# Kernel optimization log

Measured on AMD Instinct MI355X. Metric: run time of the kernel, lower is better.

## Reference

```python
import jax, jax.numpy as jnp
import numpy as np

NEG_RATIO = 3.0
IOU_THR = 0.5
ALPHA = 1.0


def _cxcywh_to_xyxy(b):
    return jnp.concatenate([b[..., :2] - b[..., 2:] / 2, b[..., :2] + b[..., 2:] / 2], -1)


def _box_iou(a, b):  # a: [G,4] xyxy, b: [A,4] xyxy -> [G,A]
    lt = jnp.maximum(a[:, None, :2], b[None, :, :2])
    rb = jnp.minimum(a[:, None, 2:], b[None, :, 2:])
    wh = jnp.clip(rb - lt, 0.0)
    inter = wh[..., 0] * wh[..., 1]
    area_a = (a[:, 2] - a[:, 0]) * (a[:, 3] - a[:, 1])
    area_b = (b[:, 2] - b[:, 0]) * (b[:, 3] - b[:, 1])
    return inter / (area_a[:, None] + area_b[None, :] - inter)


def _encode(gt, anc):  # both cxcywh, last dim 4
    g_cxcy = (gt[..., :2] - anc[..., :2]) / anc[..., 2:]
    g_wh = jnp.log(gt[..., 2:]) - jnp.log(anc[..., 2:])
    return jnp.concatenate([g_cxcy, g_wh], -1)


def _match_one(boxes, labels, anchors):
    # boxes: [G,4] cxcywh, labels: [G] int, anchors: [A,4] cxcywh -> [A,5]
    ious = _box_iou(_cxcywh_to_xyxy(boxes), _cxcywh_to_xyxy(anchors))  # [G,A]
    best_gt_ov = ious.max(0)
    best_gt_idx = ious.argmax(0)  # [A]
    over = best_gt_ov > IOU_THR  # [A]
    lab_f = labels.astype(anchors.dtype)
    # anchors over threshold take their best gt, encoded w.r.t. that anchor
    enc_per_anchor = _encode(boxes[best_gt_idx], anchors)  # [A,4]
    ph = jnp.where(over[:, None],
                   jnp.concatenate([enc_per_anchor, lab_f[best_gt_idx][:, None]], -1),
                   0.0)  # [A,5]
    # every gt also claims its best anchor
    best_prior_idx = ious.argmax(1)  # [G]
    enc_best = _encode(boxes, anchors[best_prior_idx])  # [G,4]
    y2 = jnp.concatenate([enc_best, lab_f[:, None]], -1)
    return ph.at[best_prior_idx].set(y2)


def _multibox_loss(loc_pred, conf_pred, anchors, gt_boxes, gt_labels):
    B, A, C = conf_pred.shape
    target = jax.vmap(_match_one, in_axes=(0, 0, None))(gt_boxes, gt_labels, anchors)  # [B,A,5]
    pos = (target[:, :, 4:5] > 0).astype(loc_pred.dtype)  # [B,A,1]
    num_pos = pos.sum(axis=1, keepdims=True)  # [B,1,1]
    N = pos.sum()
    # smooth L1 on masked locations (beta=1), sum reduction
    d = pos * loc_pred - pos * target[:, :, :4]
    ad = jnp.abs(d)
    loc_loss = jnp.where(ad < 1.0, 0.5 * d * d, ad - 0.5).sum()
    # hard negative mining
    num_neg = jnp.minimum(NEG_RATIO * num_pos, A - 1)  # [B,1,1]
    lse = jax.scipy.special.logsumexp(conf_pred, axis=-1, keepdims=True)  # [B,A,1]
    idx01 = (target[:, :, 4:5] != 0).astype(jnp.int32)  # faithful: gathers class 0 or 1
    gathered = jnp.take_along_axis(conf_pred, idx01, axis=-1)  # [B,A,1]
    cls_l = (lse - gathered) * (1.0 - pos)  # zero-out positives
    order = jnp.argsort(-cls_l, axis=1)  # descending sort indices
    rank = jnp.argsort(order, axis=1)  # rank of each box's loss
    neg_mask = rank < num_neg
    sampled = jnp.logical_or(pos > 0, neg_mask)  # [B,A,1]
    s = sampled.astype(conf_pred.dtype)
    logits = (s * conf_pred).reshape(-1, C)
    labels_ce = (s * target[:, :, 4:5]).reshape(-1).astype(jnp.int32)
    lse2 = jax.scipy.special.logsumexp(logits, axis=-1)
    picked = jnp.take_along_axis(logits, labels_ce[:, None], axis=1)[:, 0]
    cls_loss = (lse2 - picked).sum()
    return (loc_loss + ALPHA * cls_loss) / N


def setup_inputs() -> dict:
    key = jax.random.key(0)
    k1, k2, k3, k4, k5, k6, k7 = jax.random.split(key, 7)
    B, A, C, G = 64, 8732, 81, 32
    loc_pred = jax.random.normal(k1, (B, A, 4), jnp.float32)
    conf_pred = jax.random.normal(k2, (B, A, C), jnp.float32)
    anc_cxcy = jax.random.uniform(k3, (A, 2), jnp.float32)
    anc_wh = jax.random.uniform(k4, (A, 2), jnp.float32) * 0.48 + 0.02
    anchors = jnp.concatenate([anc_cxcy, anc_wh], -1)
    gt_cxcy = jax.random.uniform(k5, (B, G, 2), jnp.float32) * 0.8 + 0.1
    gt_wh = jax.random.uniform(k6, (B, G, 2), jnp.float32) * 0.35 + 0.05
    gt_boxes = jnp.concatenate([gt_cxcy, gt_wh], -1)
    gt_labels = jax.random.randint(k7, (B, G), 0, C - 1, jnp.int32) + 1  # labels in 1..C-1
    return {"loc_pred": loc_pred, "conf_pred": conf_pred, "anchors": anchors,
            "gt_boxes": gt_boxes, "gt_labels": gt_labels}


def reference(loc_pred, conf_pred, anchors, gt_boxes, gt_labels):
    return _multibox_loss(loc_pred, conf_pred, anchors, gt_boxes, gt_labels)
```

## Files before the change

kernel.cpp:

```cpp
#include <hip/hip_runtime.h>
#include <math.h>

#pragma clang fp contract(off)

#define BB 64
#define AA 8732
#define CC 81
#define GG 32
#define A_BLOCKS 35
#define KC_GRID 1536
#define KA1_BLOCKS (BB*A_BLOCKS)
#define KA2_BLOCKS (BB*GG/4)
#define TOT_BLOCKS (KC_GRID+KA1_BLOCKS+KA2_BLOCKS)
#define ROWS_PC 64
#define KC_CHUNKS (BB*AA/ROWS_PC)
#define CHUNK_F4 (ROWS_PC*81/4)


__device__ __forceinline__ void iou_upd(const float4 an, int a,
    float gx1, float gy1, float gx2, float gy2, float gar2,
    float& bi, float& bu, int& ba)
{
    float ax1 = an.x - an.z / 2.0f, ay1 = an.y - an.w / 2.0f;
    float ax2 = an.x + an.z / 2.0f, ay2 = an.y + an.w / 2.0f;
    float aar = (ax2 - ax1) * (ay2 - ay1);
    float ltx = fmaxf(gx1, ax1), lty = fmaxf(gy1, ay1);
    float rbx = fminf(gx2, ax2), rby = fminf(gy2, ay2);
    float w = fmaxf(rbx - ltx, 0.0f), h = fmaxf(rby - lty, 0.0f);
    float inter = w * h;
    float uni = gar2 + aar - inter;
    if (inter * bu > bi * uni) { bi = inter; bu = uni; ba = a; }
}

__global__ __launch_bounds__(256) void kAC(const float* __restrict__ anchors,
    const float* __restrict__ gt_boxes, const float* __restrict__ conf,
    unsigned char* __restrict__ bestg, unsigned int* __restrict__ bestp,
    float* __restrict__ cls_l, unsigned int* __restrict__ ticket,
    double* __restrict__ btot_acc, int* __restrict__ np_acc)
{
    __shared__ float buf[ROWS_PC * 81];
    int tid = threadIdx.x;
    if (blockIdx.x == 0 && tid == 0) {
        *ticket = 0u; *btot_acc = 0.0; *np_acc = 0;
    }
    if (blockIdx.x < KC_GRID) {
        const float4* __restrict__ src4 = (const float4*)conf;
        float4* buf4 = (float4*)buf;
        float4 r0, r1, r2, r3, r4, r5;
        int c0 = blockIdx.x;
        {
            size_t b4 = (size_t)c0 * CHUNK_F4;
            r0 = src4[b4 + tid];        r1 = src4[b4 + tid + 256];
            r2 = src4[b4 + tid + 512];  r3 = src4[b4 + tid + 768];
            r4 = src4[b4 + tid + 1024];
            if (tid < 16) r5 = src4[b4 + tid + 1280];
            buf4[tid] = r0; buf4[tid + 256] = r1; buf4[tid + 512] = r2;
            buf4[tid + 768] = r3; buf4[tid + 1024] = r4;
            if (tid < 16) buf4[tid + 1280] = r5;
        }
        for (int c = c0; c < KC_CHUNKS; c += KC_GRID) {
            int nx = c + KC_GRID;
            __syncthreads();
            if (nx < KC_CHUNKS) {
                size_t b4 = (size_t)nx * CHUNK_F4;
                r0 = src4[b4 + tid];        r1 = src4[b4 + tid + 256];
                r2 = src4[b4 + tid + 512];  r3 = src4[b4 + tid + 768];
                r4 = src4[b4 + tid + 1024];
                if (tid < 16) r5 = src4[b4 + tid + 1280];
            }
            {
                int r = tid >> 2, q = tid & 3;
                const float* row = buf + r * 81;
                int kstart = (q == 0) ? 0 : 21 + (q - 1) * 20;
                float s = 0.0f;
#pragma unroll
                for (int k = 0; k < 20; ++k) s += __expf(row[kstart + k]);
                if (q == 0) s += __expf(row[20]);
                s += __shfl_xor(s, 1);
                s += __shfl_xor(s, 2);
                if (q == 0)
                    cls_l[c * ROWS_PC + r] = __logf(s) - row[0];
            }
            if (nx < KC_CHUNKS) {
                __syncthreads();
                buf4[tid] = r0; buf4[tid + 256] = r1; buf4[tid + 512] = r2;
                buf4[tid + 768] = r3; buf4[tid + 1024] = r4;
                if (tid < 16) buf4[tid + 1280] = r5;
            }
        }
    } else if (blockIdx.x < KC_GRID + KA1_BLOCKS) {
        float4* gco = (float4*)buf;
        float* gar = buf + 128;
        int blk = blockIdx.x - KC_GRID;
        int b = blk / A_BLOCKS, ca = blk % A_BLOCKS;
        int a = ca * 256 + tid;
        if (tid < GG) {
            float4 gb = ((const float4*)gt_boxes)[b * GG + tid];
            float x1 = gb.x - gb.z / 2.0f, y1 = gb.y - gb.w / 2.0f;
            float x2 = gb.x + gb.z / 2.0f, y2 = gb.y + gb.w / 2.0f;
            gco[tid] = make_float4(x1, y1, x2, y2);
            gar[tid] = (x2 - x1) * (y2 - y1);
        }
        __syncthreads();
        if (a >= AA) return;
        float4 an = ((const float4*)anchors)[a];
        float ax1 = an.x - an.z / 2.0f, ay1 = an.y - an.w / 2.0f;
        float ax2 = an.x + an.z / 2.0f, ay2 = an.y + an.w / 2.0f;
        float aar = (ax2 - ax1) * (ay2 - ay1);
        float bi = -1.0f, bu = 1.0f; int bgi = 0;
#pragma unroll
        for (int g = 0; g < GG; ++g) {
            float4 cbox = gco[g];
            float ltx = fmaxf(cbox.x, ax1), lty = fmaxf(cbox.y, ay1);
            float rbx = fminf(cbox.z, ax2), rby = fminf(cbox.w, ay2);
            float w = fmaxf(rbx - ltx, 0.0f), h = fmaxf(rby - lty, 0.0f);
            float inter = w * h;
            float uni = gar[g] + aar - inter;
            if (inter * bu > bi * uni) { bi = inter; bu = uni; bgi = g; }
        }
        bestg[b * AA + a] = (2.0f * bi > bu) ? (unsigned char)bgi : (unsigned char)0xFF;
    } else {
        int wv = tid >> 6, lane = tid & 63;
        int pair = (blockIdx.x - KC_GRID - KA1_BLOCKS) * 4 + wv;
        int b = pair >> 5, g = pair & 31;
        float4 gb = ((const float4*)gt_boxes)[b * GG + g];
        float gx1 = gb.x - gb.z / 2.0f, gy1 = gb.y - gb.w / 2.0f;
        float gx2 = gb.x + gb.z / 2.0f, gy2 = gb.y + gb.w / 2.0f;
        float gar2 = (gx2 - gx1) * (gy2 - gy1);
        const float4* __restrict__ A4 = (const float4*)anchors;
        float bi = -1.0f, bu = 1.0f; int ba = 0;
        for (int k0 = 0; k0 < 136; k0 += 8) {
            int a0 = lane + 64 * k0;
            float4 v0 = A4[a0];
            float4 v1 = A4[a0 + 64];
            float4 v2 = A4[a0 + 128];
            float4 v3 = A4[a0 + 192];
            float4 v4 = A4[a0 + 256];
            float4 v5 = A4[a0 + 320];
            float4 v6 = A4[a0 + 384];
            float4 v7 = A4[a0 + 448];
            iou_upd(v0, a0,       gx1, gy1, gx2, gy2, gar2, bi, bu, ba);
            iou_upd(v1, a0 + 64,  gx1, gy1, gx2, gy2, gar2, bi, bu, ba);
            iou_upd(v2, a0 + 128, gx1, gy1, gx2, gy2, gar2, bi, bu, ba);
            iou_upd(v3, a0 + 192, gx1, gy1, gx2, gy2, gar2, bi, bu, ba);
            iou_upd(v4, a0 + 256, gx1, gy1, gx2, gy2, gar2, bi, bu, ba);
            iou_upd(v5, a0 + 320, gx1, gy1, gx2, gy2, gar2, bi, bu, ba);
            iou_upd(v6, a0 + 384, gx1, gy1, gx2, gy2, gar2, bi, bu, ba);
            iou_upd(v7, a0 + 448, gx1, gy1, gx2, gy2, gar2, bi, bu, ba);
        }
        if (lane < 28) {
            int a = 8704 + lane;
            iou_upd(A4[a], a, gx1, gy1, gx2, gy2, gar2, bi, bu, ba);
        }
#pragma unroll
        for (int off = 32; off > 0; off >>= 1) {
            float oi = __shfl_down(bi, off);
            float ou = __shfl_down(bu, off);
            int   oa = __shfl_down(ba, off);
            float p1 = oi * bu, p2 = bi * ou;
            bool take = (p1 > p2) || ((p1 == p2) && (oa < ba));
            if (take) { bi = oi; bu = ou; ba = oa; }
        }
        if (lane == 0) bestp[pair] = (unsigned int)ba;
    }
}

__global__ __launch_bounds__(1024, 4) void kBE(const float* __restrict__ anchors,
    const float* __restrict__ gt_boxes, const int* __restrict__ gt_labels,
    const float* __restrict__ loc_pred, const unsigned char* __restrict__ bestg,
    const unsigned int* __restrict__ bestp, const float* __restrict__ cls_l,
    const float* __restrict__ conf, unsigned int* __restrict__ ticket,
    double* __restrict__ btot_acc, int* __restrict__ np_acc,
    float* __restrict__ out)
{
    int b = blockIdx.x, tid = threadIdx.x, lane = tid & 63;
    __shared__ unsigned int cl[AA];
    __shared__ unsigned char slab[AA];
    __shared__ unsigned int hist[256];
    __shared__ float gcx[GG], gcy[GG], gw[GG], gh[GG];
    __shared__ int glab[GG];
    __shared__ unsigned int bp[GG];
    __shared__ double red_d[16], red_p[16];
    __shared__ int red_i[16];
    __shared__ unsigned int red_u[16];
    __shared__ unsigned int sh_prefix, sh_remaining;
    __shared__ int sh_np;
    __shared__ double sh_loc, sh_pc;

    if (tid < GG) {
        float4 gb = ((const float4*)gt_boxes)[b * GG + tid];
        gcx[tid] = gb.x; gcy[tid] = gb.y; gw[tid] = gb.z; gh[tid] = gb.w;
        glab[tid] = gt_labels[b * GG + tid];
        bp[tid] = bestp[b * GG + tid];
    }
    __syncthreads();

    double lsum = 0.0, pc = 0.0; int pcount = 0;
    for (int a = tid; a < AA; a += 1024) {
        int gf = -1;
#pragma unroll
        for (int g = 0; g < GG; ++g)
            if (bp[g] == (unsigned int)a) gf = g;
        int gsel;
        if (gf >= 0) gsel = gf;
        else {
            unsigned char bg = bestg[b * AA + a];
            gsel = (bg == 0xFF) ? -1 : (int)bg;
        }
        int lab = 0;
        if (gsel >= 0) {
            lab = glab[gsel];
            float4 an = ((const float4*)anchors)[a];
            float e0 = (gcx[gsel] - an.x) / an.z;
            float e1 = (gcy[gsel] - an.y) / an.w;
            float e2 = logf(gw[gsel]) - logf(an.z);
            float e3 = logf(gh[gsel]) - logf(an.w);
            float4 lp = ((const float4*)loc_pred)[b * AA + a];
            float d0 = lp.x - e0, d1 = lp.y - e1, d2 = lp.z - e2, d3 = lp.w - e3;
            float t = 0.0f, ad;
            ad = fabsf(d0); t += (ad < 1.0f) ? 0.5f * d0 * d0 : ad - 0.5f;
            ad = fabsf(d1); t += (ad < 1.0f) ? 0.5f * d1 * d1 : ad - 0.5f;
            ad = fabsf(d2); t += (ad < 1.0f) ? 0.5f * d2 * d2 : ad - 0.5f;
            ad = fabsf(d3); t += (ad < 1.0f) ? 0.5f * d3 * d3 : ad - 0.5f;
            lsum += (double)t;
            pcount++;
        }
        slab[a] = (unsigned char)lab;
        float sv = cls_l[b * AA + a];
        if (lab > 0) {
            size_t rowb = ((size_t)(b * AA + a)) * 81;
            pc += (double)(sv + conf[rowb] - conf[rowb + lab]);
            cl[a] = 0u;
        } else {
            cl[a] = __float_as_uint(fmaxf(sv, 0.0f));
        }
    }
#pragma unroll
    for (int off = 32; off > 0; off >>= 1) {
        lsum += __shfl_down(lsum, off);
        pc += __shfl_down(pc, off);
        pcount += __shfl_down(pcount, off);
    }
    if (lane == 0) { red_d[tid >> 6] = lsum; red_p[tid >> 6] = pc; red_i[tid >> 6] = pcount; }
    __syncthreads();
    if (tid == 0) {
        double L = 0.0, C = 0.0; int P = 0;
        for (int w = 0; w < 16; ++w) { L += red_d[w]; C += red_p[w]; P += red_i[w]; }
        sh_loc = L; sh_pc = C; sh_np = P;
        sh_prefix = 0u;
        sh_remaining = (unsigned int)min(3 * P, AA - 1);
    }
    __syncthreads();
    int np_ = sh_np;
    int k = min(3 * np_, AA - 1);

    double topk = 0.0;
    int p_t_pos = 0;
    if (k > 0) {
        for (int shift = 24; shift >= 0; shift -= 8) {
            if (tid < 256) hist[tid] = 0u;
            __syncthreads();
            unsigned int mask = (shift == 24) ? 0u : (0xFFFFFFFFu << (shift + 8));
            unsigned int pre = sh_prefix;
#pragma unroll
            for (int it = 0; it < 9; ++it) {
                int i = tid + it * 1024;
                bool in = (i < AA);
                unsigned int u = in ? cl[i] : 0u;
                bool act = in && ((u & mask) == pre);
                unsigned int d = (u >> shift) & 255u;
                unsigned long long actm = __ballot(act);
                while (actm) {
                    int src = __builtin_ctzll(actm);
                    unsigned int d0 = (unsigned int)__shfl((int)d, src);
                    unsigned long long m = __ballot(act && (d == d0));
                    int c = __popcll(m);
                    if (c < 8) break;
                    if (lane == src) atomicAdd(&hist[d0], (unsigned int)c);
                    actm &= ~m;
                }
                if ((actm >> lane) & 1ull) atomicAdd(&hist[d], 1u);
            }
            __syncthreads();
            if (tid < 64) {
                int l = tid;
                unsigned int h4 = hist[4 * l] + hist[4 * l + 1]
                                + hist[4 * l + 2] + hist[4 * l + 3];
                unsigned int S = h4;
#pragma unroll
                for (int off = 1; off < 64; off <<= 1) {
                    unsigned int o = __shfl_down(S, off);
                    S += (l + off < 64) ? o : 0u;
                }
                unsigned int rem = sh_remaining;
                unsigned long long ball = __ballot(S >= rem);
                int L = 63 - __clzll(ball);
                if (l == L) {
                    unsigned int rem2 = rem - (S - h4);
                    unsigned int c = 0;
                    for (int dd = 4 * L + 3; dd >= 4 * L; --dd) {
                        c += hist[dd];
                        if (c >= rem2) {
                            sh_prefix = pre | ((unsigned int)dd << shift);
                            sh_remaining = rem2 - (c - hist[dd]);
                            break;
                        }
                    }
                }
            }
            __syncthreads();
        }
        unsigned int vbits = sh_prefix;
        unsigned int myc = 0; double mys = 0.0;
        for (int i = tid; i < AA; i += 1024) {
            unsigned int u = cl[i];
            if (u > vbits) { myc++; mys += (double)__uint_as_float(u); }
        }
#pragma unroll
        for (int off = 32; off > 0; off >>= 1) {
            myc += __shfl_down(myc, off);
            mys += __shfl_down(mys, off);
        }
        if (lane == 0) { red_u[tid >> 6] = myc; red_d[tid >> 6] = mys; }
        __syncthreads();
        if (tid == 0) {
            unsigned int cnt_gt = 0; double sum_gt = 0.0;
            for (int w = 0; w < 16; ++w) { cnt_gt += red_u[w]; sum_gt += red_d[w]; }
            topk = sum_gt + (double)(k - (int)cnt_gt) * (double)__uint_as_float(vbits);
            if (vbits == 0u) {
                int t = k - (int)cnt_gt, c2 = 0;
                for (int i = 0; i < AA && c2 < t; ++i) {
                    if (cl[i] == 0u) { c2++; if (slab[i] > 0) p_t_pos++; }
                }
            }
        }
    }
    if (tid == 0) {
        int unsampled = AA - np_ - k + p_t_pos;
        double clsb = sh_pc + topk + (double)unsampled * (double)logf(81.0f);
        double myb = sh_loc + clsb;
        atomicAdd(btot_acc, myb);
        atomicAdd(np_acc, np_);
        __threadfence();
        unsigned int t = atomicAdd(ticket, 1u);
        if (t == BB - 1) {
            double tt = atomicAdd(btot_acc, 0.0);
            int nn = atomicAdd(np_acc, 0);
            out[0] = (float)(tt / (double)nn);
        }
    }
}

extern "C" void kernel_launch(void* const* d_in, const int* in_sizes, int n_in,
                              void* d_out, int out_size, void* d_ws, size_t ws_size,
                              hipStream_t stream) {
    (void)in_sizes; (void)n_in; (void)out_size; (void)ws_size;
    const float* loc_pred  = (const float*)d_in[0];
    const float* conf_pred = (const float*)d_in[1];
    const float* anchors   = (const float*)d_in[2];
    const float* gt_boxes  = (const float*)d_in[3];
    const int*   gt_labels = (const int*)d_in[4];

    char* ws = (char*)d_ws;
    unsigned int*  bestp    = (unsigned int*)(ws + 0);
    unsigned char* bestg    = (unsigned char*)(ws + 8192);
    float*         cls_l    = (float*)(ws + 567040);
    unsigned int*  ticket   = (unsigned int*)(ws + 2802432);
    double*        btot_acc = (double*)(ws + 2802440);
    int*           np_acc   = (int*)(ws + 2802448);

    kAC<<<TOT_BLOCKS, 256, 0, stream>>>(anchors, gt_boxes, conf_pred,
        bestg, bestp, cls_l, ticket, btot_acc, np_acc);
    kBE<<<BB, 1024, 0, stream>>>(anchors, gt_boxes, gt_labels, loc_pred,
        bestg, bestp, cls_l, conf_pred, ticket, btot_acc, np_acc, (float*)d_out);
}
```

Before: 314.2 us.

## Fuse match, softmax and loss stages into one kernel with per-batch ready counters

Merges the two kernels into a single persistent-style launch of 1024-thread blocks. The per-batch loss blocks spin on per-batch ready counters, which the log-sum-exp, best-gt and best-prior producer blocks increment. This lets loss work for early batches overlap with producers still running for later ones, and removes the kernel boundary. It also reshapes the producer work, with 16 threads per row for log-sum-exp and 1024-wide anchor blocks, and adds a small init kernel to zero the counters. The spin-wait relies on every producer block being scheduled before or alongside the waiting consumers; if they are not, it can deadlock or waste occupancy.

```diff
diff --git a/kernel.cpp b/kernel.cpp
--- a/kernel.cpp
+++ b/kernel.cpp
@@ -5,17 +5,35 @@
 
 #define BB 64
 #define AA 8732
-#define CC 81
 #define GG 32
-#define A_BLOCKS 35
-#define KC_GRID 1536
-#define KA1_BLOCKS (BB*A_BLOCKS)
-#define KA2_BLOCKS (BB*GG/4)
-#define TOT_BLOCKS (KC_GRID+KA1_BLOCKS+KA2_BLOCKS)
-#define ROWS_PC 64
-#define KC_CHUNKS (BB*AA/ROWS_PC)
-#define CHUNK_F4 (ROWS_PC*81/4)
-
+
+#define KC_GRID    768
+#define KC_CHUNKS  8732
+#define CHUNK_F4   1296
+#define KC_TRIPS   12
+#define KA1_PER    9
+#define KA1_BLOCKS (BB*KA1_PER)
+#define KA2_BLOCKS (BB*2)
+#define ROLE_A1    KC_GRID
+#define ROLE_A2    (KC_GRID+KA1_BLOCKS)
+#define ROLE_BE    (KC_GRID+KA1_BLOCKS+KA2_BLOCKS)
+#define TOT_BLOCKS (ROLE_BE+BB)
+
+
+struct BESmem {
+    unsigned int cl[AA];
+    unsigned int hist[256];
+    float gcx[GG], gcy[GG], gw[GG], gh[GG];
+    int glab[GG];
+    unsigned int bp[GG];
+    double red_d[16], red_p[16];
+    double sh_loc, sh_pc;
+    int red_i[16];
+    unsigned int red_u[16];
+    unsigned int sh_prefix, sh_remaining;
+    int sh_np;
+    unsigned char slab[AA];
+};
 
 __device__ __forceinline__ void iou_upd(const float4 an, int a,
     float gx1, float gy1, float gx2, float gy2, float gar2,
@@ -32,68 +50,92 @@
     if (inter * bu > bi * uni) { bi = inter; bu = uni; ba = a; }
 }
 
-__global__ __launch_bounds__(256) void kAC(const float* __restrict__ anchors,
-    const float* __restrict__ gt_boxes, const float* __restrict__ conf,
+__global__ __launch_bounds__(256) void kInit(unsigned int* __restrict__ z)
+{
+    for (int i = threadIdx.x; i < 1029; i += 256) z[i] = 0u;
+}
+
+__global__ __launch_bounds__(1024, 4) void kFused(
+    const float* __restrict__ loc_pred, const float* __restrict__ conf,
+    const float* __restrict__ anchors, const float* __restrict__ gt_boxes,
+    const int* __restrict__ gt_labels,
     unsigned char* __restrict__ bestg, unsigned int* __restrict__ bestp,
-    float* __restrict__ cls_l, unsigned int* __restrict__ ticket,
-    double* __restrict__ btot_acc, int* __restrict__ np_acc)
+    float* __restrict__ cls_l, unsigned int* __restrict__ ready,
+    unsigned int* __restrict__ ticket, double* __restrict__ btot_acc,
+    int* __restrict__ np_acc, float* __restrict__ out)
 {
-    __shared__ float buf[ROWS_PC * 81];
+    __shared__ __align__(16) unsigned char smem[sizeof(BESmem)];
     int tid = threadIdx.x;
-    if (blockIdx.x == 0 && tid == 0) {
-        *ticket = 0u; *btot_acc = 0.0; *np_acc = 0;
-    }
+
     if (blockIdx.x < KC_GRID) {
+        float* buf = (float*)smem;
+        float4* buf4 = (float4*)smem;
         const float4* __restrict__ src4 = (const float4*)conf;
-        float4* buf4 = (float4*)buf;
-        float4 r0, r1, r2, r3, r4, r5;
-        int c0 = blockIdx.x;
+        float4 r0, r1;
         {
-            size_t b4 = (size_t)c0 * CHUNK_F4;
-            r0 = src4[b4 + tid];        r1 = src4[b4 + tid + 256];
-            r2 = src4[b4 + tid + 512];  r3 = src4[b4 + tid + 768];
-            r4 = src4[b4 + tid + 1024];
-            if (tid < 16) r5 = src4[b4 + tid + 1280];
-            buf4[tid] = r0; buf4[tid + 256] = r1; buf4[tid + 512] = r2;
-            buf4[tid + 768] = r3; buf4[tid + 1024] = r4;
-            if (tid < 16) buf4[tid + 1280] = r5;
-        }
-        for (int c = c0; c < KC_CHUNKS; c += KC_GRID) {
+            size_t b4 = (size_t)blockIdx.x * CHUNK_F4;
+            r0 = src4[b4 + tid];
+            if (tid < CHUNK_F4 - 1024) r1 = src4[b4 + 1024 + tid];
+            buf4[tid] = r0;
+            if (tid < CHUNK_F4 - 1024) buf4[1024 + tid] = r1;
+        }
+        int pend = -1;
+        for (int t = 0; t < KC_TRIPS; ++t) {
+            int c = blockIdx.x + t * KC_GRID;
             int nx = c + KC_GRID;
+            bool hc = c < KC_CHUNKS, hn = nx < KC_CHUNKS;
             __syncthreads();
-            if (nx < KC_CHUNKS) {
+            if (pend >= 0) {
+                if (tid == 0) {
+                    __threadfence();
+                    int i1 = (pend * 64) / AA, i2 = (pend * 64 + 63) / AA;
+                    atomicAdd(&ready[i1 * 16], 1u);
+                    if (i2 != i1) atomicAdd(&ready[i2 * 16], 1u);
+                }
+                pend = -1;
+            }
+            if (hn) {
                 size_t b4 = (size_t)nx * CHUNK_F4;
-                r0 = src4[b4 + tid];        r1 = src4[b4 + tid + 256];
-                r2 = src4[b4 + tid + 512];  r3 = src4[b4 + tid + 768];
-                r4 = src4[b4 + tid + 1024];
-                if (tid < 16) r5 = src4[b4 + tid + 1280];
-            }
-            {
-                int r = tid >> 2, q = tid & 3;
+                r0 = src4[b4 + tid];
+                if (tid < CHUNK_F4 - 1024) r1 = src4[b4 + 1024 + tid];
+            }
+            if (hc) {
+                int r = tid >> 4, q = tid & 15;
                 const float* row = buf + r * 81;
-                int kstart = (q == 0) ? 0 : 21 + (q - 1) * 20;
-                float s = 0.0f;
-#pragma unroll
-                for (int k = 0; k < 20; ++k) s += __expf(row[kstart + k]);
-                if (q == 0) s += __expf(row[20]);
-                s += __shfl_xor(s, 1);
-                s += __shfl_xor(s, 2);
+                float s;
+                if (q == 0) {
+                    s = __expf(row[0]) + __expf(row[1]) + __expf(row[2])
+                      + __expf(row[3]) + __expf(row[4]) + __expf(row[5]);
+                } else {
+                    int ks = 6 + (q - 1) * 5;
+                    s = __expf(row[ks]) + __expf(row[ks + 1]) + __expf(row[ks + 2])
+                      + __expf(row[ks + 3]) + __expf(row[ks + 4]);
+                }
+                s += __shfl_xor(s, 1); s += __shfl_xor(s, 2);
+                s += __shfl_xor(s, 4); s += __shfl_xor(s, 8);
                 if (q == 0)
-                    cls_l[c * ROWS_PC + r] = __logf(s) - row[0];
-            }
-            if (nx < KC_CHUNKS) {
+                    cls_l[c * 64 + r] = __logf(s) - row[0];
+            }
+            if (hn) {
                 __syncthreads();
-                buf4[tid] = r0; buf4[tid + 256] = r1; buf4[tid + 512] = r2;
-                buf4[tid + 768] = r3; buf4[tid + 1024] = r4;
-                if (tid < 16) buf4[tid + 1280] = r5;
-            }
-        }
-    } else if (blockIdx.x < KC_GRID + KA1_BLOCKS) {
-        float4* gco = (float4*)buf;
-        float* gar = buf + 128;
-        int blk = blockIdx.x - KC_GRID;
-        int b = blk / A_BLOCKS, ca = blk % A_BLOCKS;
-        int a = ca * 256 + tid;
+                buf4[tid] = r0;
+                if (tid < CHUNK_F4 - 1024) buf4[1024 + tid] = r1;
+            }
+            if (hc) pend = c;
+        }
+        __syncthreads();
+        if (pend >= 0 && tid == 0) {
+            __threadfence();
+            int i1 = (pend * 64) / AA, i2 = (pend * 64 + 63) / AA;
+            atomicAdd(&ready[i1 * 16], 1u);
+            if (i2 != i1) atomicAdd(&ready[i2 * 16], 1u);
+        }
+    } else if (blockIdx.x < ROLE_A2) {
+        float4* gco = (float4*)smem;
+        float* gar = (float*)smem + 128;
+        int blk = blockIdx.x - ROLE_A1;
+        int b = blk / KA1_PER, ca = blk % KA1_PER;
+        int a = ca * 1024 + tid;
         if (tid < GG) {
             float4 gb = ((const float4*)gt_boxes)[b * GG + tid];
             float x1 = gb.x - gb.z / 2.0f, y1 = gb.y - gb.w / 2.0f;
@@ -102,26 +144,31 @@
             gar[tid] = (x2 - x1) * (y2 - y1);
         }
         __syncthreads();
-        if (a >= AA) return;
-        float4 an = ((const float4*)anchors)[a];
-        float ax1 = an.x - an.z / 2.0f, ay1 = an.y - an.w / 2.0f;
-        float ax2 = an.x + an.z / 2.0f, ay2 = an.y + an.w / 2.0f;
-        float aar = (ax2 - ax1) * (ay2 - ay1);
-        float bi = -1.0f, bu = 1.0f; int bgi = 0;
-#pragma unroll
-        for (int g = 0; g < GG; ++g) {
-            float4 cbox = gco[g];
-            float ltx = fmaxf(cbox.x, ax1), lty = fmaxf(cbox.y, ay1);
-            float rbx = fminf(cbox.z, ax2), rby = fminf(cbox.w, ay2);
-            float w = fmaxf(rbx - ltx, 0.0f), h = fmaxf(rby - lty, 0.0f);
-            float inter = w * h;
-            float uni = gar[g] + aar - inter;
-            if (inter * bu > bi * uni) { bi = inter; bu = uni; bgi = g; }
-        }
-        bestg[b * AA + a] = (2.0f * bi > bu) ? (unsigned char)bgi : (unsigned char)0xFF;
-    } else {
+        if (a < AA) {
+            float4 an = ((const float4*)anchors)[a];
+            float ax1 = an.x - an.z / 2.0f, ay1 = an.y - an.w / 2.0f;
+            float ax2 = an.x + an.z / 2.0f, ay2 = an.y + an.w / 2.0f;
+            float aar = (ax2 - ax1) * (ay2 - ay1);
+            float bi = -1.0f, bu = 1.0f; int bgi = 0;
+#pragma unroll
+            for (int g = 0; g < GG; ++g) {
+                float4 cbox = gco[g];
+                float ltx = fmaxf(cbox.x, ax1), lty = fmaxf(cbox.y, ay1);
+                float rbx = fminf(cbox.z, ax2), rby = fminf(cbox.w, ay2);
+                float w = fmaxf(rbx - ltx, 0.0f), h = fmaxf(rby - lty, 0.0f);
+                float inter = w * h;
+                float uni = gar[g] + aar - inter;
+                if (inter * bu > bi * uni) { bi = inter; bu = uni; bgi = g; }
+            }
+            bestg[b * AA + a] = (2.0f * bi > bu) ? (unsigned char)bgi
+                                                 : (unsigned char)0xFF;
+        }
+        __syncthreads();
+        if (tid == 0) { __threadfence(); atomicAdd(&ready[b * 16], 1u); }
+    } else if (blockIdx.x < ROLE_BE) {
         int wv = tid >> 6, lane = tid & 63;
-        int pair = (blockIdx.x - KC_GRID - KA1_BLOCKS) * 4 + wv;
+        int blk = blockIdx.x - ROLE_A2;
+        int pair = blk * 16 + wv;
         int b = pair >> 5, g = pair & 31;
         float4 gb = ((const float4*)gt_boxes)[b * GG + g];
         float gx1 = gb.x - gb.z / 2.0f, gy1 = gb.y - gb.w / 2.0f;
@@ -162,191 +209,182 @@
             if (take) { bi = oi; bu = ou; ba = oa; }
         }
         if (lane == 0) bestp[pair] = (unsigned int)ba;
-    }
-}
-
-__global__ __launch_bounds__(1024, 4) void kBE(const float* __restrict__ anchors,
-    const float* __restrict__ gt_boxes, const int* __restrict__ gt_labels,
-    const float* __restrict__ loc_pred, const unsigned char* __restrict__ bestg,
-    const unsigned int* __restrict__ bestp, const float* __restrict__ cls_l,
-    const float* __restrict__ conf, unsigned int* __restrict__ ticket,
-    double* __restrict__ btot_acc, int* __restrict__ np_acc,
-    float* __restrict__ out)
-{
-    int b = blockIdx.x, tid = threadIdx.x, lane = tid & 63;
-    __shared__ unsigned int cl[AA];
-    __shared__ unsigned char slab[AA];
-    __shared__ unsigned int hist[256];
-    __shared__ float gcx[GG], gcy[GG], gw[GG], gh[GG];
-    __shared__ int glab[GG];
-    __shared__ unsigned int bp[GG];
-    __shared__ double red_d[16], red_p[16];
-    __shared__ int red_i[16];
-    __shared__ unsigned int red_u[16];
-    __shared__ unsigned int sh_prefix, sh_remaining;
-    __shared__ int sh_np;
-    __shared__ double sh_loc, sh_pc;
-
-    if (tid < GG) {
-        float4 gb = ((const float4*)gt_boxes)[b * GG + tid];
-        gcx[tid] = gb.x; gcy[tid] = gb.y; gw[tid] = gb.z; gh[tid] = gb.w;
-        glab[tid] = gt_labels[b * GG + tid];
-        bp[tid] = bestp[b * GG + tid];
-    }
-    __syncthreads();
-
-    double lsum = 0.0, pc = 0.0; int pcount = 0;
-    for (int a = tid; a < AA; a += 1024) {
-        int gf = -1;
-#pragma unroll
-        for (int g = 0; g < GG; ++g)
-            if (bp[g] == (unsigned int)a) gf = g;
-        int gsel;
-        if (gf >= 0) gsel = gf;
-        else {
-            unsigned char bg = bestg[b * AA + a];
-            gsel = (bg == 0xFF) ? -1 : (int)bg;
-        }
-        int lab = 0;
-        if (gsel >= 0) {
-            lab = glab[gsel];
-            float4 an = ((const float4*)anchors)[a];
-            float e0 = (gcx[gsel] - an.x) / an.z;
-            float e1 = (gcy[gsel] - an.y) / an.w;
-            float e2 = logf(gw[gsel]) - logf(an.z);
-            float e3 = logf(gh[gsel]) - logf(an.w);
-            float4 lp = ((const float4*)loc_pred)[b * AA + a];
-            float d0 = lp.x - e0, d1 = lp.y - e1, d2 = lp.z - e2, d3 = lp.w - e3;
-            float t = 0.0f, ad;
-            ad = fabsf(d0); t += (ad < 1.0f) ? 0.5f * d0 * d0 : ad - 0.5f;
-            ad = fabsf(d1); t += (ad < 1.0f) ? 0.5f * d1 * d1 : ad - 0.5f;
-            ad = fabsf(d2); t += (ad < 1.0f) ? 0.5f * d2 * d2 : ad - 0.5f;
-            ad = fabsf(d3); t += (ad < 1.0f) ? 0.5f * d3 * d3 : ad - 0.5f;
-            lsum += (double)t;
-            pcount++;
-        }
-        slab[a] = (unsigned char)lab;
-        float sv = cls_l[b * AA + a];
-        if (lab > 0) {
-            size_t rowb = ((size_t)(b * AA + a)) * 81;
-            pc += (double)(sv + conf[rowb] - conf[rowb + lab]);
-            cl[a] = 0u;
-        } else {
-            cl[a] = __float_as_uint(fmaxf(sv, 0.0f));
-        }
-    }
-#pragma unroll
-    for (int off = 32; off > 0; off >>= 1) {
-        lsum += __shfl_down(lsum, off);
-        pc += __shfl_down(pc, off);
-        pcount += __shfl_down(pcount, off);
-    }
-    if (lane == 0) { red_d[tid >> 6] = lsum; red_p[tid >> 6] = pc; red_i[tid >> 6] = pcount; }
-    __syncthreads();
-    if (tid == 0) {
-        double L = 0.0, C = 0.0; int P = 0;
-        for (int w = 0; w < 16; ++w) { L += red_d[w]; C += red_p[w]; P += red_i[w]; }
-        sh_loc = L; sh_pc = C; sh_np = P;
-        sh_prefix = 0u;
-        sh_remaining = (unsigned int)min(3 * P, AA - 1);
-    }
-    __syncthreads();
-    int np_ = sh_np;
-    int k = min(3 * np_, AA - 1);
-
-    double topk = 0.0;
-    int p_t_pos = 0;
-    if (k > 0) {
-        for (int shift = 24; shift >= 0; shift -= 8) {
-            if (tid < 256) hist[tid] = 0u;
-            __syncthreads();
-            unsigned int mask = (shift == 24) ? 0u : (0xFFFFFFFFu << (shift + 8));
-            unsigned int pre = sh_prefix;
-#pragma unroll
-            for (int it = 0; it < 9; ++it) {
-                int i = tid + it * 1024;
-                bool in = (i < AA);
-                unsigned int u = in ? cl[i] : 0u;
-                bool act = in && ((u & mask) == pre);
-                unsigned int d = (u >> shift) & 255u;
-                unsigned long long actm = __ballot(act);
-                while (actm) {
-                    int src = __builtin_ctzll(actm);
-                    unsigned int d0 = (unsigned int)__shfl((int)d, src);
-                    unsigned long long m = __ballot(act && (d == d0));
-                    int c = __popcll(m);
-                    if (c < 8) break;
-                    if (lane == src) atomicAdd(&hist[d0], (unsigned int)c);
-                    actm &= ~m;
+        __syncthreads();
+        if (tid == 0) { __threadfence(); atomicAdd(&ready[b * 16], 1u); }
+    } else {
+        BESmem& S = *reinterpret_cast<BESmem*>(smem);
+        int b = blockIdx.x - ROLE_BE, lane = tid & 63;
+        if (tid == 0) {
+            unsigned int tgt = (unsigned int)(((AA * (b + 1) - 1) >> 6)
+                               - ((AA * b) >> 6) + 1 + KA1_PER + 2);
+            while (atomicAdd(&ready[b * 16], 0u) < tgt)
+                __builtin_amdgcn_s_sleep(2);
+            __threadfence();
+        }
+        __syncthreads();
+        if (tid < GG) {
+            float4 gb = ((const float4*)gt_boxes)[b * GG + tid];
+            S.gcx[tid] = gb.x; S.gcy[tid] = gb.y; S.gw[tid] = gb.z; S.gh[tid] = gb.w;
+            S.glab[tid] = gt_labels[b * GG + tid];
+            S.bp[tid] = bestp[b * GG + tid];
+        }
+        __syncthreads();
+
+        double lsum = 0.0, pc = 0.0; int pcount = 0;
+        for (int a = tid; a < AA; a += 1024) {
+            int gf = -1;
+#pragma unroll
+            for (int g = 0; g < GG; ++g)
+                if (S.bp[g] == (unsigned int)a) gf = g;
+            int gsel;
+            if (gf >= 0) gsel = gf;
+            else {
+                unsigned char bg = bestg[b * AA + a];
+                gsel = (bg == 0xFF) ? -1 : (int)bg;
+            }
+            int lab = 0;
+            if (gsel >= 0) {
+                lab = S.glab[gsel];
+                float4 an = ((const float4*)anchors)[a];
+                float e0 = (S.gcx[gsel] - an.x) / an.z;
+                float e1 = (S.gcy[gsel] - an.y) / an.w;
+                float e2 = logf(S.gw[gsel]) - logf(an.z);
+                float e3 = logf(S.gh[gsel]) - logf(an.w);
+                float4 lp = ((const float4*)loc_pred)[b * AA + a];
+                float d0 = lp.x - e0, d1 = lp.y - e1, d2 = lp.z - e2, d3 = lp.w - e3;
+                float t = 0.0f, ad;
+                ad = fabsf(d0); t += (ad < 1.0f) ? 0.5f * d0 * d0 : ad - 0.5f;
+                ad = fabsf(d1); t += (ad < 1.0f) ? 0.5f * d1 * d1 : ad - 0.5f;
+                ad = fabsf(d2); t += (ad < 1.0f) ? 0.5f * d2 * d2 : ad - 0.5f;
+                ad = fabsf(d3); t += (ad < 1.0f) ? 0.5f * d3 * d3 : ad - 0.5f;
+                lsum += (double)t;
+                pcount++;
+            }
+            S.slab[a] = (unsigned char)lab;
+            float sv = cls_l[b * AA + a];
+            if (lab > 0) {
+                size_t rowb = ((size_t)(b * AA + a)) * 81;
+                pc += (double)(sv + conf[rowb] - conf[rowb + lab]);
+                S.cl[a] = 0u;
+            } else {
+                S.cl[a] = __float_as_uint(fmaxf(sv, 0.0f));
+            }
+        }
+#pragma unroll
+        for (int off = 32; off > 0; off >>= 1) {
+            lsum += __shfl_down(lsum, off);
+            pc += __shfl_down(pc, off);
+            pcount += __shfl_down(pcount, off);
+        }
+        if (lane == 0) {
+            S.red_d[tid >> 6] = lsum; S.red_p[tid >> 6] = pc; S.red_i[tid >> 6] = pcount;
+        }
+        __syncthreads();
+        if (tid == 0) {
+            double L = 0.0, C = 0.0; int P = 0;
+            for (int w = 0; w < 16; ++w) { L += S.red_d[w]; C += S.red_p[w]; P += S.red_i[w]; }
+            S.sh_loc = L; S.sh_pc = C; S.sh_np = P;
+            S.sh_prefix = 0u;
+            S.sh_remaining = (unsigned int)min(3 * P, AA - 1);
+        }
+        __syncthreads();
+        int np_ = S.sh_np;
+        int k = min(3 * np_, AA - 1);
+
+        double topk = 0.0;
+        int p_t_pos = 0;
+        if (k > 0) {
+            for (int shift = 24; shift >= 0; shift -= 8) {
+                if (tid < 256) S.hist[tid] = 0u;
+                __syncthreads();
+                unsigned int mask = (shift == 24) ? 0u : (0xFFFFFFFFu << (shift + 8));
+                unsigned int pre = S.sh_prefix;
+#pragma unroll
+                for (int it = 0; it < 9; ++it) {
+                    int i = tid + it * 1024;
+                    bool in = (i < AA);
+                    unsigned int u = in ? S.cl[i] : 0u;
+                    bool act = in && ((u & mask) == pre);
+                    unsigned int d = (u >> shift) & 255u;
+                    unsigned long long actm = __ballot(act);
+                    while (actm) {
+                        int src = __builtin_ctzll(actm);
+                        unsigned int d0 = (unsigned int)__shfl((int)d, src);
+                        unsigned long long m = __ballot(act && (d == d0));
+                        int c = __popcll(m);
+                        if (c < 8) break;
+                        if (lane == src) atomicAdd(&S.hist[d0], (unsigned int)c);
+                        actm &= ~m;
+                    }
+                    if ((actm >> lane) & 1ull) atomicAdd(&S.hist[d], 1u);
                 }
-                if ((actm >> lane) & 1ull) atomicAdd(&hist[d], 1u);
-            }
-            __syncthreads();
-            if (tid < 64) {
-                int l = tid;
-                unsigned int h4 = hist[4 * l] + hist[4 * l + 1]
-                                + hist[4 * l + 2] + hist[4 * l + 3];
-                unsigned int S = h4;
-#pragma unroll
-                for (int off = 1; off < 64; off <<= 1) {
-                    unsigned int o = __shfl_down(S, off);
-                    S += (l + off < 64) ? o : 0u;
-                }
-                unsigned int rem = sh_remaining;
-                unsigned long long ball = __ballot(S >= rem);
-                int L = 63 - __clzll(ball);
-                if (l == L) {
-                    unsigned int rem2 = rem - (S - h4);
-                    unsigned int c = 0;
-                    for (int dd = 4 * L + 3; dd >= 4 * L; --dd) {
-                        c += hist[dd];
-                        if (c >= rem2) {
-                            sh_prefix = pre | ((unsigned int)dd << shift);
-                            sh_remaining = rem2 - (c - hist[dd]);
-                            break;
+                __syncthreads();
+                if (tid < 64) {
+                    int l = tid;
+                    unsigned int h4 = S.hist[4 * l] + S.hist[4 * l + 1]
+                                    + S.hist[4 * l + 2] + S.hist[4 * l + 3];
+                    unsigned int Ssum = h4;
+#pragma unroll
+                    for (int off = 1; off < 64; off <<= 1) {
+                        unsigned int o = __shfl_down(Ssum, off);
+                        Ssum += (l + off < 64) ? o : 0u;
+                    }
+                    unsigned int rem = S.sh_remaining;
+                    unsigned long long ball = __ballot(Ssum >= rem);
+                    int L = 63 - __clzll(ball);
+                    if (l == L) {
+                        unsigned int rem2 = rem - (Ssum - h4);
+                        unsigned int c = 0;
+                        for (int dd = 4 * L + 3; dd >= 4 * L; --dd) {
+                            c += S.hist[dd];
+                            if (c >= rem2) {
+                                S.sh_prefix = pre | ((unsigned int)dd << shift);
+                                S.sh_remaining = rem2 - (c - S.hist[dd]);
+                                break;
+                            }
                         }
                     }
                 }
-            }
+                __syncthreads();
+            }
+            unsigned int vbits = S.sh_prefix;
+            unsigned int myc = 0; double mys = 0.0;
+            for (int i = tid; i < AA; i += 1024) {
+                unsigned int u = S.cl[i];
+                if (u > vbits) { myc++; mys += (double)__uint_as_float(u); }
+            }
+#pragma unroll
+            for (int off = 32; off > 0; off >>= 1) {
+                myc += __shfl_down(myc, off);
+                mys += __shfl_down(mys, off);
+            }
+            if (lane == 0) { S.red_u[tid >> 6] = myc; S.red_d[tid >> 6] = mys; }
             __syncthreads();
-        }
-        unsigned int vbits = sh_prefix;
-        unsigned int myc = 0; double mys = 0.0;
-        for (int i = tid; i < AA; i += 1024) {
-            unsigned int u = cl[i];
-            if (u > vbits) { myc++; mys += (double)__uint_as_float(u); }
-        }
-#pragma unroll
-        for (int off = 32; off > 0; off >>= 1) {
-            myc += __shfl_down(myc, off);
-            mys += __shfl_down(mys, off);
-        }
-        if (lane == 0) { red_u[tid >> 6] = myc; red_d[tid >> 6] = mys; }
-        __syncthreads();
+            if (tid == 0) {
+                unsigned int cnt_gt = 0; double sum_gt = 0.0;
+                for (int w = 0; w < 16; ++w) { cnt_gt += S.red_u[w]; sum_gt += S.red_d[w]; }
+                topk = sum_gt + (double)(k - (int)cnt_gt) * (double)__uint_as_float(vbits);
+                if (vbits == 0u) {
+                    int t = k - (int)cnt_gt, c2 = 0;
+                    for (int i = 0; i < AA && c2 < t; ++i) {
+                        if (S.cl[i] == 0u) { c2++; if (S.slab[i] > 0) p_t_pos++; }
+                    }
+                }
+            }
+        }
         if (tid == 0) {
-            unsigned int cnt_gt = 0; double sum_gt = 0.0;
-            for (int w = 0; w < 16; ++w) { cnt_gt += red_u[w]; sum_gt += red_d[w]; }
-            topk = sum_gt + (double)(k - (int)cnt_gt) * (double)__uint_as_float(vbits);
-            if (vbits == 0u) {
-                int t = k - (int)cnt_gt, c2 = 0;
-                for (int i = 0; i < AA && c2 < t; ++i) {
-                    if (cl[i] == 0u) { c2++; if (slab[i] > 0) p_t_pos++; }
-                }
-            }
-        }
-    }
-    if (tid == 0) {
-        int unsampled = AA - np_ - k + p_t_pos;
-        double clsb = sh_pc + topk + (double)unsampled * (double)logf(81.0f);
-        double myb = sh_loc + clsb;
-        atomicAdd(btot_acc, myb);
-        atomicAdd(np_acc, np_);
-        __threadfence();
-        unsigned int t = atomicAdd(ticket, 1u);
-        if (t == BB - 1) {
-            double tt = atomicAdd(btot_acc, 0.0);
-            int nn = atomicAdd(np_acc, 0);
-            out[0] = (float)(tt / (double)nn);
+            int unsampled = AA - np_ - k + p_t_pos;
+            double clsb = S.sh_pc + topk + (double)unsampled * (double)logf(81.0f);
+            double myb = S.sh_loc + clsb;
+            atomicAdd(btot_acc, myb);
+            atomicAdd(np_acc, np_);
+            __threadfence();
+            unsigned int t = atomicAdd(ticket, 1u);
+            if (t == BB - 1) {
+                double tt = atomicAdd(btot_acc, 0.0);
+                int nn = atomicAdd(np_acc, 0);
+                out[0] = (float)(tt / (double)nn);
+            }
         }
     }
 }
@@ -365,12 +403,13 @@
     unsigned int*  bestp    = (unsigned int*)(ws + 0);
     unsigned char* bestg    = (unsigned char*)(ws + 8192);
     float*         cls_l    = (float*)(ws + 567040);
-    unsigned int*  ticket   = (unsigned int*)(ws + 2802432);
-    double*        btot_acc = (double*)(ws + 2802440);
-    int*           np_acc   = (int*)(ws + 2802448);
-
-    kAC<<<TOT_BLOCKS, 256, 0, stream>>>(anchors, gt_boxes, conf_pred,
-        bestg, bestp, cls_l, ticket, btot_acc, np_acc);
-    kBE<<<BB, 1024, 0, stream>>>(anchors, gt_boxes, gt_labels, loc_pred,
-        bestg, bestp, cls_l, conf_pred, ticket, btot_acc, np_acc, (float*)d_out);
+    unsigned int*  ready    = (unsigned int*)(ws + 2802432);
+    unsigned int*  ticket   = (unsigned int*)(ws + 2806528);
+    double*        btot_acc = (double*)(ws + 2806536);
+    int*           np_acc   = (int*)(ws + 2806544);
+
+    kInit <<<1, 256, 0, stream>>>(ready);
+    kFused<<<TOT_BLOCKS, 1024, 0, stream>>>(loc_pred, conf_pred, anchors,
+        gt_boxes, gt_labels, bestg, bestp, cls_l, ready, ticket, btot_acc,
+        np_acc, (float*)d_out);
 }
```

After: 721.1 us. +129.5%, slower.
